# Optimization experiments

Hardware: AMD Instinct MI355X
Metric: run time of the kernel (lower is better)

The kernel has to match this reference:

```python
import jax, jax.numpy as jnp
import numpy as np

N = 50000      # nodes
E = 800000     # edges
DIN = 128      # input feature dim
H = 4          # heads
D = 16         # per-head output dim
NEG_SLOPE = 0.2


def setup_inputs() -> dict:
    key = jax.random.key(0)
    k1, k2, k3, k4, k5, k6 = jax.random.split(key, 6)
    h = jax.random.normal(k1, (N, DIN), dtype=jnp.float32)
    W = jax.random.normal(k2, (DIN, H * D), dtype=jnp.float32) * 0.05
    attn_l = jax.random.normal(k3, (H, D), dtype=jnp.float32) * 0.1
    attn_r = jax.random.normal(k4, (H, D), dtype=jnp.float32) * 0.1
    src = jax.random.randint(k5, (E,), 0, N, dtype=jnp.int32)
    dst = jax.random.randint(k6, (E,), 0, N, dtype=jnp.int32)
    return {"h": h, "W": W, "attn_l": attn_l, "attn_r": attn_r, "src": src, "dst": dst}


def reference(h, W, attn_l, attn_r, src, dst):
    n = h.shape[0]
    # linear projection: [N, H, D]
    feat = (h @ W).reshape(n, H, D)
    # per-node attention halves: [N, H]
    el = jnp.einsum('nhd,hd->nh', feat, attn_l)
    er = jnp.einsum('nhd,hd->nh', feat, attn_r)
    # per-edge logits: [E, H]
    e = jax.nn.leaky_relu(el[src] + er[dst], negative_slope=NEG_SLOPE)
    # segment softmax grouped by destination node
    m = jax.ops.segment_max(e, dst, num_segments=n)          # [N, H]
    ex = jnp.exp(e - m[dst])                                  # [E, H]
    denom = jax.ops.segment_sum(ex, dst, num_segments=n)     # [N, H]
    a = ex / denom[dst]                                       # [E, H]
    # weighted aggregation of source features: [E, H, D] -> [N, H, D]
    msg = a[:, :, None] * feat[src]
    out = jax.ops.segment_sum(msg, dst, num_segments=n)
    # mean over heads (the wrapper's .mean(1)): [N, D]
    return out.mean(axis=1)
```

## Files before the change

### kernel.cpp

```cpp
#include <hip/hip_runtime.h>
#include <hip/hip_fp16.h>

#define NN   50000
#define EE   800000
#define KDIN 128
#define NH   4
#define ND   16
#define NEG_SLOPE 0.2f

#define NB        196
#define CAP       5120
#define NNODE_PAD (NB * 256)
#define PROJ_ROWS 32
#define PROJ_LDP  130

__device__ __forceinline__ float lrelu(float x) {
    return x > 0.f ? x : NEG_SLOPE * x;
}
__device__ __forceinline__ float h2f(unsigned short u) {
    return __half2float(__ushort_as_half(u));
}

__global__ __launch_bounds__(256) void k_proj(
    const float* __restrict__ h, const float* __restrict__ W,
    const float* __restrict__ attn_l, const float* __restrict__ attn_r,
    unsigned short* __restrict__ feat_h, float* __restrict__ el, float* __restrict__ er,
    int* __restrict__ gcur)
{
    __shared__ float4 Wl[KDIN * 16];
    __shared__ float  hrow[PROJ_ROWS * PROJ_LDP];

    const int tid = threadIdx.x;
    if (blockIdx.x == 0) gcur[tid] = 0;

    const float4* W4 = (const float4*)W;
    #pragma unroll
    for (int i = 0; i < 8; ++i) Wl[tid + 256 * i] = W4[tid + 256 * i];

    const int row_base = blockIdx.x * PROJ_ROWS;

    {
        const float4* h4 = (const float4*)h;
        #pragma unroll
        for (int i = 0; i < 4; ++i) {
            const int idx = tid + 256 * i;
            const int r   = idx >> 5;
            const int c   = idx & 31;
            int gr = row_base + r;
            if (gr >= NN) gr = NN - 1;
            float4 v = h4[(size_t)gr * 32 + c];
            *(float4*)&hrow[r * PROJ_LDP + c * 4] = v;
        }
    }
    __syncthreads();

    const int c4 = tid & 15;
    const int rg = tid >> 4;
    const float* row0 = &hrow[(rg * 2    ) * PROJ_LDP];
    const float* row1 = &hrow[(rg * 2 + 1) * PROJ_LDP];

    float4 a0 = make_float4(0.f, 0.f, 0.f, 0.f);
    float4 a1 = make_float4(0.f, 0.f, 0.f, 0.f);
    #pragma unroll 8
    for (int k = 0; k < KDIN; ++k) {
        const float4 w  = Wl[k * 16 + c4];
        const float  h0 = row0[k];
        const float  h1 = row1[k];
        a0.x = fmaf(h0, w.x, a0.x);
        a0.y = fmaf(h0, w.y, a0.y);
        a0.z = fmaf(h0, w.z, a0.z);
        a0.w = fmaf(h0, w.w, a0.w);
        a1.x = fmaf(h1, w.x, a1.x);
        a1.y = fmaf(h1, w.y, a1.y);
        a1.z = fmaf(h1, w.z, a1.z);
        a1.w = fmaf(h1, w.w, a1.w);
    }

    const int r0 = row_base + rg * 2;
    const int r1 = r0 + 1;

    ushort4 v0, v1;
    v0.x = __half_as_ushort(__float2half_rn(a0.x));
    v0.y = __half_as_ushort(__float2half_rn(a0.y));
    v0.z = __half_as_ushort(__float2half_rn(a0.z));
    v0.w = __half_as_ushort(__float2half_rn(a0.w));
    v1.x = __half_as_ushort(__float2half_rn(a1.x));
    v1.y = __half_as_ushort(__float2half_rn(a1.y));
    v1.z = __half_as_ushort(__float2half_rn(a1.z));
    v1.w = __half_as_ushort(__float2half_rn(a1.w));
    if (r0 < NN) ((ushort4*)feat_h)[(size_t)r0 * 16 + c4] = v0;
    if (r1 < NN) ((ushort4*)feat_h)[(size_t)r1 * 16 + c4] = v1;

    const float4 al = ((const float4*)attn_l)[c4];
    const float4 ar = ((const float4*)attn_r)[c4];
    float pl0 = a0.x*al.x + a0.y*al.y + a0.z*al.z + a0.w*al.w;
    float pr0 = a0.x*ar.x + a0.y*ar.y + a0.z*ar.z + a0.w*ar.w;
    float pl1 = a1.x*al.x + a1.y*al.y + a1.z*al.z + a1.w*al.w;
    float pr1 = a1.x*ar.x + a1.y*ar.y + a1.z*ar.z + a1.w*ar.w;
    pl0 += __shfl_xor(pl0, 1); pl0 += __shfl_xor(pl0, 2);
    pr0 += __shfl_xor(pr0, 1); pr0 += __shfl_xor(pr0, 2);
    pl1 += __shfl_xor(pl1, 1); pl1 += __shfl_xor(pl1, 2);
    pr1 += __shfl_xor(pr1, 1); pr1 += __shfl_xor(pr1, 2);
    if ((c4 & 3) == 0) {
        const int head = c4 >> 2;
        if (r0 < NN) { el[r0 * NH + head] = pl0; er[r0 * NH + head] = pr0; }
        if (r1 < NN) { el[r1 * NH + head] = pl1; er[r1 * NH + head] = pr1; }
    }
}

__global__ __launch_bounds__(256) void k_part(
    const int* __restrict__ src, const int* __restrict__ dst,
    int* __restrict__ gcur, unsigned int* __restrict__ pairs)
{
    __shared__ int lhist[NB];
    const int tid = threadIdx.x;
    const int eb  = blockIdx.x * 1280;

    unsigned int preg[5];
    int breg[5];
    if (tid < NB) lhist[tid] = 0;
    __syncthreads();

    #pragma unroll
    for (int j = 0; j < 5; ++j) {
        const int e = eb + j * 256 + tid;
        const int d = dst[e];
        const int s = src[e];
        breg[j] = d >> 8;
        preg[j] = (unsigned int)s | ((unsigned int)(d & 255) << 16);
        atomicAdd(&lhist[breg[j]], 1);
    }
    __syncthreads();

    if (tid < NB) lhist[tid] = atomicAdd(&gcur[tid], lhist[tid]);
    __syncthreads();

    #pragma unroll
    for (int j = 0; j < 5; ++j) {
        const int b   = breg[j];
        const int idx = atomicAdd(&lhist[b], 1);
        if (idx < CAP) pairs[b * CAP + idx] = preg[j];
    }
}

__global__ __launch_bounds__(512) void k_lsort(
    const int* __restrict__ gcur, const unsigned int* __restrict__ pairs,
    unsigned short* __restrict__ sorted_src,
    int* __restrict__ row_start, int* __restrict__ degv)
{
    __shared__ unsigned int buf[CAP];
    __shared__ int lhist[256];
    __shared__ int lpre[256];
    const int tid = threadIdx.x;
    const int b   = blockIdx.x;
    const int n   = min(gcur[b], CAP);

    if (tid < 256) lhist[tid] = 0;
    __syncthreads();

    for (int i = tid; i < n; i += 512) {
        const unsigned int p = pairs[b * CAP + i];
        buf[i] = p;
        atomicAdd(&lhist[(p >> 16) & 255], 1);
    }
    __syncthreads();

    if (tid < 256) lpre[tid] = lhist[tid];
    __syncthreads();
    #pragma unroll
    for (int off = 1; off < 256; off <<= 1) {
        int v = 0;
        if (tid < 256 && tid >= off) v = lpre[tid - off];
        __syncthreads();
        if (tid < 256) lpre[tid] += v;
        __syncthreads();
    }

    if (tid < 256) {
        const int node = b * 256 + tid;
        const int excl = lpre[tid] - lhist[tid];
        row_start[node] = b * CAP + excl;
        degv[node]      = lhist[tid];
        lhist[tid]      = excl;
    }
    __syncthreads();

    for (int i = tid; i < n; i += 512) {
        const unsigned int p = buf[i];
        const int r = atomicAdd(&lhist[(p >> 16) & 255], 1);
        sorted_src[b * CAP + r] = (unsigned short)(p & 0xFFFFu);
    }
}

__global__ __launch_bounds__(256) void k_gather(
    const float* __restrict__ el, const float* __restrict__ er,
    const unsigned short* __restrict__ feat_h,
    const unsigned short* __restrict__ sorted_src,
    const int* __restrict__ row_start, const int* __restrict__ degv,
    float* __restrict__ out)
{
    const int tid = threadIdx.x;
    const int t   = blockIdx.x * 4 + (tid >> 6);
    if (t >= NN) return;
    const int lane = tid & 63;
    const int hd   = lane >> 4;
    const int base = row_start[t];
    const int n    = degv[t];
    const float er_h = er[t * NH + hd];

    float acc = 0.f, dsum = 0.f;
    int j = 0;
    for (; j + 4 <= n; j += 4) {
        const int s0 = (int)sorted_src[base + j + 0];
        const int s1 = (int)sorted_src[base + j + 1];
        const int s2 = (int)sorted_src[base + j + 2];
        const int s3 = (int)sorted_src[base + j + 3];
        const float x0 = el[s0 * NH + hd] + er_h;
        const float x1 = el[s1 * NH + hd] + er_h;
        const float x2 = el[s2 * NH + hd] + er_h;
        const float x3 = el[s3 * NH + hd] + er_h;
        const float f0 = h2f(feat_h[(size_t)s0 * 64 + lane]);
        const float f1 = h2f(feat_h[(size_t)s1 * 64 + lane]);
        const float f2 = h2f(feat_h[(size_t)s2 * 64 + lane]);
        const float f3 = h2f(feat_h[(size_t)s3 * 64 + lane]);
        const float e0 = __expf(lrelu(x0));
        const float e1 = __expf(lrelu(x1));
        const float e2 = __expf(lrelu(x2));
        const float e3 = __expf(lrelu(x3));
        dsum += (e0 + e1) + (e2 + e3);
        acc = fmaf(e0, f0, acc);
        acc = fmaf(e1, f1, acc);
        acc = fmaf(e2, f2, acc);
        acc = fmaf(e3, f3, acc);
    }
    for (; j < n; ++j) {
        const int s = (int)sorted_src[base + j];
        const float x  = el[s * NH + hd] + er_h;
        const float fv = h2f(feat_h[(size_t)s * 64 + lane]);
        const float ex = __expf(lrelu(x));
        dsum += ex;
        acc = fmaf(ex, fv, acc);
    }

    float r = (n > 0) ? acc * __builtin_amdgcn_rcpf(dsum) : 0.f;
    r += __shfl_xor(r, 16);
    r += __shfl_xor(r, 32);
    if (lane < 16) out[t * ND + lane] = 0.25f * r;
}

extern "C" void kernel_launch(void* const* d_in, const int* in_sizes, int n_in,
                              void* d_out, int out_size, void* d_ws, size_t ws_size,
                              hipStream_t stream)
{
    const float* h  = (const float*)d_in[0];
    const float* W  = (const float*)d_in[1];
    const float* al = (const float*)d_in[2];
    const float* ar = (const float*)d_in[3];
    const int* src  = (const int*)d_in[4];
    const int* dst  = (const int*)d_in[5];
    float* out = (float*)d_out;

    unsigned short* feat_h = (unsigned short*)d_ws;
    float* el   = (float*)(feat_h + (size_t)NN * 64);
    float* er   = el + (size_t)NN * NH;
    int*   gcur = (int*)(er + (size_t)NN * NH);
    unsigned int* pairs = (unsigned int*)(gcur + 256);
    unsigned short* ssrc = (unsigned short*)(pairs + (size_t)NB * CAP);
    int*   row_start = (int*)(ssrc + (size_t)NB * CAP);
    int*   degv      = row_start + NNODE_PAD;

    const int proj_blocks = (NN + PROJ_ROWS - 1) / PROJ_ROWS;
    k_proj  <<<proj_blocks, 256, 0, stream>>>(h, W, al, ar, feat_h, el, er, gcur);
    k_part  <<<EE / 1280,   256, 0, stream>>>(src, dst, gcur, pairs);
    k_lsort <<<NB,          512, 0, stream>>>(gcur, pairs, ssrc, row_start, degv);
    k_gather<<<NN / 4,      256, 0, stream>>>(el, er, feat_h, ssrc, row_start, degv, out);
}
```

Measured before the change: 153.5 us.

## Use smaller dst buckets, pack row info, batch-8 gather with masked tail

Halves the destination bucket size (128 nodes, 391 buckets), so k_lsort runs more, smaller blocks with less shared memory and a shorter scan. Row start and degree are packed into one 32-bit word, so the gather does one metadata load instead of two. The gather loop now issues 8 source-index, el and feature loads at a time with a clamped, masked tail instead of a 4-wide loop plus scalar remainder, to raise memory-level parallelism. Risks: degree is capped at 255 by the 8-bit field, the smaller CAP leaves less room for bucket overflow, and the tail does up to 7 wasted loads per node.

Result: no change. 152.7 us (-0.5%).

```diff
diff --git a/kernel.cpp b/kernel.cpp
--- a/kernel.cpp
+++ b/kernel.cpp
@@ -8,9 +8,10 @@
 #define ND   16
 #define NEG_SLOPE 0.2f
 
-#define NB        196
-#define CAP       5120
-#define NNODE_PAD (NB * 256)
+#define NB        391
+#define NBIN      128
+#define CAP       2560
+#define NNODE_PAD (NB * NBIN)
 #define PROJ_ROWS 32
 #define PROJ_LDP  130
 
@@ -31,7 +32,7 @@
     __shared__ float  hrow[PROJ_ROWS * PROJ_LDP];
 
     const int tid = threadIdx.x;
-    if (blockIdx.x == 0) gcur[tid] = 0;
+    if (blockIdx.x == 0) { gcur[tid] = 0; gcur[tid + 256] = 0; }
 
     const float4* W4 = (const float4*)W;
     #pragma unroll
@@ -118,7 +119,7 @@
 
     unsigned int preg[5];
     int breg[5];
-    if (tid < NB) lhist[tid] = 0;
+    for (int i = tid; i < NB; i += 256) lhist[i] = 0;
     __syncthreads();
 
     #pragma unroll
@@ -126,13 +127,13 @@
         const int e = eb + j * 256 + tid;
         const int d = dst[e];
         const int s = src[e];
-        breg[j] = d >> 8;
-        preg[j] = (unsigned int)s | ((unsigned int)(d & 255) << 16);
+        breg[j] = d >> 7;
+        preg[j] = (unsigned int)s | ((unsigned int)(d & 127) << 16);
         atomicAdd(&lhist[breg[j]], 1);
     }
     __syncthreads();
 
-    if (tid < NB) lhist[tid] = atomicAdd(&gcur[tid], lhist[tid]);
+    for (int i = tid; i < NB; i += 256) lhist[i] = atomicAdd(&gcur[i], lhist[i]);
     __syncthreads();
 
     #pragma unroll
@@ -145,49 +146,48 @@
 
 __global__ __launch_bounds__(512) void k_lsort(
     const int* __restrict__ gcur, const unsigned int* __restrict__ pairs,
-    unsigned short* __restrict__ sorted_src,
-    int* __restrict__ row_start, int* __restrict__ degv)
+    unsigned short* __restrict__ sorted_src, unsigned int* __restrict__ rowinfo)
 {
     __shared__ unsigned int buf[CAP];
-    __shared__ int lhist[256];
-    __shared__ int lpre[256];
+    __shared__ int lhist[NBIN];
+    __shared__ int lpre[NBIN];
     const int tid = threadIdx.x;
     const int b   = blockIdx.x;
     const int n   = min(gcur[b], CAP);
 
-    if (tid < 256) lhist[tid] = 0;
+    if (tid < NBIN) lhist[tid] = 0;
     __syncthreads();
 
     for (int i = tid; i < n; i += 512) {
         const unsigned int p = pairs[b * CAP + i];
         buf[i] = p;
-        atomicAdd(&lhist[(p >> 16) & 255], 1);
-    }
-    __syncthreads();
-
-    if (tid < 256) lpre[tid] = lhist[tid];
-    __syncthreads();
-    #pragma unroll
-    for (int off = 1; off < 256; off <<= 1) {
+        atomicAdd(&lhist[(p >> 16) & 127], 1);
+    }
+    __syncthreads();
+
+    if (tid < NBIN) lpre[tid] = lhist[tid];
+    __syncthreads();
+    #pragma unroll
+    for (int off = 1; off < NBIN; off <<= 1) {
         int v = 0;
-        if (tid < 256 && tid >= off) v = lpre[tid - off];
+        if (tid < NBIN && tid >= off) v = lpre[tid - off];
         __syncthreads();
-        if (tid < 256) lpre[tid] += v;
+        if (tid < NBIN) lpre[tid] += v;
         __syncthreads();
     }
 
-    if (tid < 256) {
-        const int node = b * 256 + tid;
-        const int excl = lpre[tid] - lhist[tid];
-        row_start[node] = b * CAP + excl;
-        degv[node]      = lhist[tid];
-        lhist[tid]      = excl;
+    if (tid < NBIN) {
+        const int node = b * NBIN + tid;
+        const int cnt  = lhist[tid];
+        const int excl = lpre[tid] - cnt;
+        rowinfo[node] = ((unsigned int)(b * CAP + excl) << 8) | (unsigned int)cnt;
+        lhist[tid]    = excl;
     }
     __syncthreads();
 
     for (int i = tid; i < n; i += 512) {
         const unsigned int p = buf[i];
-        const int r = atomicAdd(&lhist[(p >> 16) & 255], 1);
+        const int r = atomicAdd(&lhist[(p >> 16) & 127], 1);
         sorted_src[b * CAP + r] = (unsigned short)(p & 0xFFFFu);
     }
 }
@@ -196,50 +196,38 @@
     const float* __restrict__ el, const float* __restrict__ er,
     const unsigned short* __restrict__ feat_h,
     const unsigned short* __restrict__ sorted_src,
-    const int* __restrict__ row_start, const int* __restrict__ degv,
+    const unsigned int* __restrict__ rowinfo,
     float* __restrict__ out)
 {
-    const int tid = threadIdx.x;
-    const int t   = blockIdx.x * 4 + (tid >> 6);
-    if (t >= NN) return;
+    const int tid  = threadIdx.x;
+    const int t    = blockIdx.x * 4 + (tid >> 6);
     const int lane = tid & 63;
     const int hd   = lane >> 4;
-    const int base = row_start[t];
-    const int n    = degv[t];
+
+    const unsigned int info = rowinfo[t];
+    const int base = (int)(info >> 8);
+    const int n    = (int)(info & 255u);
     const float er_h = er[t * NH + hd];
 
     float acc = 0.f, dsum = 0.f;
-    int j = 0;
-    for (; j + 4 <= n; j += 4) {
-        const int s0 = (int)sorted_src[base + j + 0];
-        const int s1 = (int)sorted_src[base + j + 1];
-        const int s2 = (int)sorted_src[base + j + 2];
-        const int s3 = (int)sorted_src[base + j + 3];
-        const float x0 = el[s0 * NH + hd] + er_h;
-        const float x1 = el[s1 * NH + hd] + er_h;
-        const float x2 = el[s2 * NH + hd] + er_h;
-        const float x3 = el[s3 * NH + hd] + er_h;
-        const float f0 = h2f(feat_h[(size_t)s0 * 64 + lane]);
-        const float f1 = h2f(feat_h[(size_t)s1 * 64 + lane]);
-        const float f2 = h2f(feat_h[(size_t)s2 * 64 + lane]);
-        const float f3 = h2f(feat_h[(size_t)s3 * 64 + lane]);
-        const float e0 = __expf(lrelu(x0));
-        const float e1 = __expf(lrelu(x1));
-        const float e2 = __expf(lrelu(x2));
-        const float e3 = __expf(lrelu(x3));
-        dsum += (e0 + e1) + (e2 + e3);
-        acc = fmaf(e0, f0, acc);
-        acc = fmaf(e1, f1, acc);
-        acc = fmaf(e2, f2, acc);
-        acc = fmaf(e3, f3, acc);
-    }
-    for (; j < n; ++j) {
-        const int s = (int)sorted_src[base + j];
-        const float x  = el[s * NH + hd] + er_h;
-        const float fv = h2f(feat_h[(size_t)s * 64 + lane]);
-        const float ex = __expf(lrelu(x));
-        dsum += ex;
-        acc = fmaf(ex, fv, acc);
+    for (int j = 0; j < n; j += 8) {
+        const int rem = n - j;
+        int sq[8];
+        #pragma unroll
+        for (int q = 0; q < 8; ++q)
+            sq[q] = (int)sorted_src[base + min(j + q, n - 1)];
+        float xq[8], fq[8];
+        #pragma unroll
+        for (int q = 0; q < 8; ++q) xq[q] = el[sq[q] * NH + hd];
+        #pragma unroll
+        for (int q = 0; q < 8; ++q) fq[q] = h2f(feat_h[(size_t)sq[q] * 64 + lane]);
+        #pragma unroll
+        for (int q = 0; q < 8; ++q) {
+            float e = __expf(lrelu(xq[q] + er_h));
+            e = (q < rem) ? e : 0.f;
+            dsum += e;
+            acc = fmaf(e, fq[q], acc);
+        }
     }
 
     float r = (n > 0) ? acc * __builtin_amdgcn_rcpf(dsum) : 0.f;
@@ -264,14 +252,13 @@
     float* el   = (float*)(feat_h + (size_t)NN * 64);
     float* er   = el + (size_t)NN * NH;
     int*   gcur = (int*)(er + (size_t)NN * NH);
-    unsigned int* pairs = (unsigned int*)(gcur + 256);
+    unsigned int* pairs = (unsigned int*)(gcur + 512);
     unsigned short* ssrc = (unsigned short*)(pairs + (size_t)NB * CAP);
-    int*   row_start = (int*)(ssrc + (size_t)NB * CAP);
-    int*   degv      = row_start + NNODE_PAD;
+    unsigned int* rowinfo = (unsigned int*)(ssrc + (size_t)NB * CAP);
 
     const int proj_blocks = (NN + PROJ_ROWS - 1) / PROJ_ROWS;
     k_proj  <<<proj_blocks, 256, 0, stream>>>(h, W, al, ar, feat_h, el, er, gcur);
     k_part  <<<EE / 1280,   256, 0, stream>>>(src, dst, gcur, pairs);
-    k_lsort <<<NB,          512, 0, stream>>>(gcur, pairs, ssrc, row_start, degv);
-    k_gather<<<NN / 4,      256, 0, stream>>>(el, er, feat_h, ssrc, row_start, degv, out);
-}
+    k_lsort <<<NB,          512, 0, stream>>>(gcur, pairs, ssrc, rowinfo);
+    k_gather<<<NN / 4,      256, 0, stream>>>(el, er, feat_h, ssrc, rowinfo, out);
+}
```
